# Performance work log

Hardware: AMD Instinct MI355X
Metric: run time of the kernel (lower is better)

Reference implementation:

```python
import jax, jax.numpy as jnp
import numpy as np

N_NODES = 75000
N_EDGES = 1200000
DIM = 64


def setup_inputs() -> dict:
    key = jax.random.key(0)
    ks = jax.random.split(key, 9)
    d_u = jax.random.normal(ks[0], (N_NODES, DIM), dtype=jnp.float32)
    p_u = jax.random.normal(ks[1], (N_NODES, DIM), dtype=jnp.float32)
    s = 1.0 / np.sqrt(DIM)
    w_q = jax.random.normal(ks[2], (DIM, DIM), dtype=jnp.float32) * s
    w_k = jax.random.normal(ks[3], (DIM, DIM), dtype=jnp.float32) * s
    w_v = jax.random.normal(ks[4], (DIM, DIM), dtype=jnp.float32) * s
    e1 = jax.random.normal(ks[5], (DIM,), dtype=jnp.float32) * s
    e2 = jax.random.normal(ks[6], (DIM,), dtype=jnp.float32) * s
    src = jax.random.randint(ks[7], (N_EDGES,), 0, N_NODES, dtype=jnp.int32)
    dst = jax.random.randint(ks[8], (N_EDGES,), 0, N_NODES, dtype=jnp.int32)
    return {"d_u": d_u, "p_u": p_u, "w_q": w_q, "w_k": w_k, "w_v": w_v,
            "e1": e1, "e2": e2, "src": src, "dst": dst}


def reference(d_u, p_u, w_q, w_k, w_v, e1, e2, src, dst):
    n_nodes = d_u.shape[0]
    # per-node edge scores: e1(w_k(p_u)) on src side, e2(w_q(d_u)) on dst side
    h_src = (p_u @ w_k.T) @ e1            # [N]
    h_dst = (d_u @ w_q.T) @ e2            # [N]
    # apply_edges(u_add_v): c_e = h_src[u] + h_dst[v], shape [E]
    c = h_src[src] + h_dst[dst]
    # EdgeWeightNorm(norm='right'): divide by sum of incoming edge weights at dst
    denom = jax.ops.segment_sum(c, dst, num_segments=n_nodes)  # [N]
    c = c / denom[dst]
    # update_all(u_mul_e, sum): messages w_v(p_u)[u] * c_e, summed at dst
    wv = p_u @ w_v.T                      # [N, D]
    msg = wv[src] * c[:, None]            # [E, D]
    out = jax.ops.segment_sum(msg, dst, num_segments=n_nodes)  # [N, D]
    return out
```

## Files before the change

### kernel.cpp

```cpp
#include <hip/hip_runtime.h>

#define N_NODES 75000
#define N_EDGES 1200000
#define DIM 64
#define SCAN_BLK 1024
#define N_SCAN_BLKS ((N_NODES + SCAN_BLK - 1) / SCAN_BLK)
#define NCOPY 8
#define HIST_BLKS ((N_EDGES + 1023) / 1024)

__device__ __forceinline__ float lane_bcf(float v, int l) {
    return __int_as_float(__builtin_amdgcn_readlane(__float_as_int(v), l));
}
__device__ __forceinline__ int lane_bci(int v, int l) {
    return __builtin_amdgcn_readlane(v, l);
}

__global__ void vec_precompute(const float* __restrict__ w_q,
                               const float* __restrict__ w_k,
                               const float* __restrict__ e1,
                               const float* __restrict__ e2,
                               double* __restrict__ a,
                               double* __restrict__ b) {
    int t = threadIdx.x;
    if (t < DIM) {
        double s = 0.0;
        #pragma unroll
        for (int j = 0; j < DIM; ++j) s += (double)e1[j] * (double)w_k[j * DIM + t];
        a[t] = s;
    } else if (t < 2 * DIM) {
        int d = t - DIM;
        double s = 0.0;
        #pragma unroll
        for (int j = 0; j < DIM; ++j) s += (double)e2[j] * (double)w_q[j * DIM + d];
        b[d] = s;
    }
}

__global__ __launch_bounds__(256, 4) void node_wave(
    const float* __restrict__ d_u, const float* __restrict__ p_u,
    const float* __restrict__ w_v,
    const double* __restrict__ a_vec, const double* __restrict__ b_vec,
    double* __restrict__ h_src, double* __restrict__ h_dst,
    float* __restrict__ wv_out) {
    int lane = threadIdx.x & 63;
    int wave = (blockIdx.x * 256 + threadIdx.x) >> 6;
    int nwaves = gridDim.x * 4;

    float w[DIM];
    const float4* wr = (const float4*)(w_v + (size_t)lane * DIM);
    #pragma unroll
    for (int k = 0; k < DIM / 4; ++k) {
        float4 v = wr[k];
        w[4 * k + 0] = v.x; w[4 * k + 1] = v.y;
        w[4 * k + 2] = v.z; w[4 * k + 3] = v.w;
    }
    double al = a_vec[lane];
    double bl = b_vec[lane];

    for (int i = wave; i < N_NODES; i += nwaves) {
        float pl = p_u[(size_t)i * DIM + lane];
        float dl = d_u[(size_t)i * DIM + lane];

        double hs = (double)pl * al;
        #pragma unroll
        for (int off = 32; off > 0; off >>= 1) hs += __shfl_xor(hs, off, 64);
        double hd = (double)dl * bl;
        #pragma unroll
        for (int off = 32; off > 0; off >>= 1) hd += __shfl_xor(hd, off, 64);
        if (lane == 0) { h_src[i] = hs; h_dst[i] = hd; }

        float a0 = 0.f, a1 = 0.f, a2 = 0.f, a3 = 0.f;
        #pragma unroll
        for (int d = 0; d < DIM; d += 4) {
            a0 += w[d + 0] * lane_bcf(pl, d + 0);
            a1 += w[d + 1] * lane_bcf(pl, d + 1);
            a2 += w[d + 2] * lane_bcf(pl, d + 2);
            a3 += w[d + 3] * lane_bcf(pl, d + 3);
        }
        wv_out[(size_t)i * DIM + lane] = (a0 + a1) + (a2 + a3);
    }
}

__global__ __launch_bounds__(256) void hist_kernel(
    const int* __restrict__ dst, int* __restrict__ cnt8,
    int* __restrict__ rank) {
    int base = blockIdx.x << 10;
    int* mycnt = cnt8 + (size_t)(blockIdx.x & (NCOPY - 1)) * N_NODES;
    #pragma unroll
    for (int k = 0; k < 4; ++k) {
        int e = base + k * 256 + threadIdx.x;
        if (e < N_EDGES) rank[e] = atomicAdd(&mycnt[dst[e]], 1);
    }
}

__global__ __launch_bounds__(SCAN_BLK) void scan1_kernel(
    int* __restrict__ cnt8, int* __restrict__ cnt,
    int* __restrict__ row, int* __restrict__ bsum) {
    __shared__ int sh[SCAN_BLK];
    int tid = threadIdx.x;
    int i = blockIdx.x * SCAN_BLK + tid;
    int v = 0;
    if (i < N_NODES) {
        int run = 0;
        #pragma unroll
        for (int c = 0; c < NCOPY; ++c) {
            int x = cnt8[(size_t)c * N_NODES + i];
            cnt8[(size_t)c * N_NODES + i] = run;
            run += x;
        }
        v = run;
        cnt[i] = run;
    }
    sh[tid] = v;
    __syncthreads();
    for (int off = 1; off < SCAN_BLK; off <<= 1) {
        int t = (tid >= off) ? sh[tid - off] : 0;
        __syncthreads();
        sh[tid] += t;
        __syncthreads();
    }
    if (i < N_NODES) row[i] = sh[tid] - v;
    if (tid == SCAN_BLK - 1) bsum[blockIdx.x] = sh[tid];
}

__global__ __launch_bounds__(256) void scan23_kernel(
    int* __restrict__ row, const int* __restrict__ bsum) {
    __shared__ int pref[N_SCAN_BLKS];
    int tid = threadIdx.x;
    if (tid == 0) {
        int run = 0;
        #pragma unroll 8
        for (int k = 0; k < N_SCAN_BLKS; ++k) { pref[k] = run; run += bsum[k]; }
    }
    __syncthreads();
    int i = blockIdx.x * 256 + tid;
    if (i >= N_NODES) return;
    row[i] += pref[i / SCAN_BLK];
}

__global__ __launch_bounds__(256) void build_kernel(
    const int* __restrict__ src, const int* __restrict__ dst,
    const int* __restrict__ row, const int* __restrict__ cnt8,
    const int* __restrict__ rank, int* __restrict__ csr_src) {
    int e = blockIdx.x * 256 + threadIdx.x;
    if (e >= N_EDGES) return;
    int d = dst[e];
    int copy = (e >> 10) & (NCOPY - 1);
    int pos = row[d] + cnt8[(size_t)copy * N_NODES + d] + rank[e];
    csr_src[pos] = src[e];
}

__global__ __launch_bounds__(256) void node_gather(
    const int* __restrict__ row, const int* __restrict__ cnt,
    const int* __restrict__ csr_src,
    const double* __restrict__ h_src, const double* __restrict__ h_dst,
    const float* __restrict__ wv, float* __restrict__ out) {
    int gtid = blockIdx.x * 256 + threadIdx.x;
    int node = gtid >> 6;
    int lane = threadIdx.x & 63;
    if (node >= N_NODES) return;

    int start = row[node];
    int deg = cnt[node];
    double hd = h_dst[node];

    if (deg <= 64) {
        int s0 = 0;
        double c0 = 0.0;
        if (lane < deg) {
            s0 = csr_src[start + lane];
            c0 = h_src[s0] + hd;
        }
        double r = c0;
        if (deg > 32) r += __shfl_xor(r, 32, 64);
        if (deg > 16) r += __shfl_xor(r, 16, 64);
        r += __shfl_xor(r, 8, 64);
        r += __shfl_xor(r, 4, 64);
        r += __shfl_xor(r, 2, 64);
        r += __shfl_xor(r, 1, 64);
        double inv = 1.0 / r;
        float cf0 = (lane < deg) ? (float)(c0 * inv) : 0.f;

        int g = lane >> 4;
        int sub = lane & 15;
        float ax = 0.f, ay = 0.f, az = 0.f, aw = 0.f;
        int rounds = (deg + 3) >> 2;
        int j = 0;
        for (; j + 2 <= rounds; j += 2) {
            int l0 = 4 * j + g;
            int l1 = l0 + 4;
            int   sA = __shfl(s0, l0, 64);
            float cA = __shfl(cf0, l0, 64);
            int   sB = __shfl(s0, l1, 64);
            float cB = __shfl(cf0, l1, 64);
            float4 vA = ((const float4*)(wv + (size_t)sA * DIM))[sub];
            float4 vB = ((const float4*)(wv + (size_t)sB * DIM))[sub];
            ax += vA.x * cA; ay += vA.y * cA; az += vA.z * cA; aw += vA.w * cA;
            ax += vB.x * cB; ay += vB.y * cB; az += vB.z * cB; aw += vB.w * cB;
        }
        if (j < rounds) {
            int l0 = 4 * j + g;
            int   sA = __shfl(s0, l0, 64);
            float cA = __shfl(cf0, l0, 64);
            float4 vA = ((const float4*)(wv + (size_t)sA * DIM))[sub];
            ax += vA.x * cA; ay += vA.y * cA; az += vA.z * cA; aw += vA.w * cA;
        }
        ax += __shfl_xor(ax, 16, 64); ay += __shfl_xor(ay, 16, 64);
        az += __shfl_xor(az, 16, 64); aw += __shfl_xor(aw, 16, 64);
        ax += __shfl_xor(ax, 32, 64); ay += __shfl_xor(ay, 32, 64);
        az += __shfl_xor(az, 32, 64); aw += __shfl_xor(aw, 32, 64);
        if (g == 0) {
            float4 o; o.x = ax; o.y = ay; o.z = az; o.w = aw;
            ((float4*)(out + (size_t)node * DIM))[sub] = o;
        }
    } else {
        double denom = 0.0;
        for (int base = 0; base < deg; base += 64) {
            int m = deg - base; if (m > 64) m = 64;
            double c = 0.0;
            if (lane < m) {
                int s = csr_src[start + base + lane];
                c = h_src[s] + hd;
            }
            #pragma unroll
            for (int off = 32; off > 0; off >>= 1) c += __shfl_xor(c, off, 64);
            denom += c;
        }
        double inv = 1.0 / denom;
        float acc = 0.f;
        for (int base = 0; base < deg; base += 64) {
            int m = deg - base; if (m > 64) m = 64;
            int s1 = 0; float cf1 = 0.f;
            if (lane < m) {
                s1 = csr_src[start + base + lane];
                cf1 = (float)((h_src[s1] + hd) * inv);
            }
            for (int j = 0; j < m; ++j) {
                int s = lane_bci(s1, j);
                float cf = lane_bcf(cf1, j);
                acc += wv[(size_t)s * DIM + lane] * cf;
            }
        }
        out[(size_t)node * DIM + lane] = acc;
    }
}

extern "C" void kernel_launch(void* const* d_in, const int* in_sizes, int n_in,
                              void* d_out, int out_size, void* d_ws, size_t ws_size,
                              hipStream_t stream) {
    const float* d_u = (const float*)d_in[0];
    const float* p_u = (const float*)d_in[1];
    const float* w_q = (const float*)d_in[2];
    const float* w_k = (const float*)d_in[3];
    const float* w_v = (const float*)d_in[4];
    const float* e1  = (const float*)d_in[5];
    const float* e2  = (const float*)d_in[6];
    const int*   src = (const int*)d_in[7];
    const int*   dst = (const int*)d_in[8];
    float* out = (float*)d_out;

    double* a      = (double*)d_ws;
    double* b      = a + DIM;
    double* h_src  = b + DIM;
    double* h_dst  = h_src + N_NODES;
    float*  wv     = (float*)(h_dst + N_NODES);
    int*    cnt    = (int*)(wv + (size_t)N_NODES * DIM);
    int*    row    = cnt + N_NODES;
    int*    bsum   = row + N_NODES;
    int*    cnt8   = bsum + 128;
    int*    rank   = cnt8 + (size_t)NCOPY * N_NODES;
    int*    csr_src= rank + N_EDGES;

    vec_precompute<<<1, 128, 0, stream>>>(w_q, w_k, e1, e2, a, b);

    hipMemsetAsync(cnt8, 0, sizeof(int) * (size_t)NCOPY * N_NODES, stream);

    hist_kernel<<<HIST_BLKS, 256, 0, stream>>>(dst, cnt8, rank);

    node_wave<<<1024, 256, 0, stream>>>(
        d_u, p_u, w_v, a, b, h_src, h_dst, wv);

    scan1_kernel<<<N_SCAN_BLKS, SCAN_BLK, 0, stream>>>(cnt8, cnt, row, bsum);
    scan23_kernel<<<(N_NODES + 255) / 256, 256, 0, stream>>>(row, bsum);

    build_kernel<<<(N_EDGES + 255) / 256, 256, 0, stream>>>(
        src, dst, row, cnt8, rank, csr_src);

    node_gather<<<(N_NODES * 64 + 255) / 256, 256, 0, stream>>>(
        row, cnt, csr_src, h_src, h_dst, wv, out);
}
```

Measured before the change: 255.8 us.

## Fuse histogram, node projection and vector precompute into one launch

Merges the edge histogram kernel and the per-node projection kernel into one grid, with block-index ranges selecting the role. The tiny vec_precompute kernel is removed, and each wave now recomputes its a/b dot-product coefficients inline from w_k, w_q, e1 and e2. This removes two kernel launches and lets the atomic-heavy histogram overlap with the bandwidth-bound node projection. In exchange every node wave does redundant 64-term double-precision reductions, and the histogram blocks now run under the fat kernel's launch bounds and register budget.

```diff
diff --git a/kernel.cpp b/kernel.cpp
--- a/kernel.cpp
+++ b/kernel.cpp
@@ -7,6 +7,8 @@
 #define N_SCAN_BLKS ((N_NODES + SCAN_BLK - 1) / SCAN_BLK)
 #define NCOPY 8
 #define HIST_BLKS ((N_EDGES + 1023) / 1024)
+#define NW_BLKS 1024
+#define FAT_BLKS (HIST_BLKS + NW_BLKS)
 
 __device__ __forceinline__ float lane_bcf(float v, int l) {
     return __int_as_float(__builtin_amdgcn_readlane(__float_as_int(v), l));
@@ -15,36 +17,36 @@
     return __builtin_amdgcn_readlane(v, l);
 }
 
-__global__ void vec_precompute(const float* __restrict__ w_q,
-                               const float* __restrict__ w_k,
-                               const float* __restrict__ e1,
-                               const float* __restrict__ e2,
-                               double* __restrict__ a,
-                               double* __restrict__ b) {
-    int t = threadIdx.x;
-    if (t < DIM) {
-        double s = 0.0;
-        #pragma unroll
-        for (int j = 0; j < DIM; ++j) s += (double)e1[j] * (double)w_k[j * DIM + t];
-        a[t] = s;
-    } else if (t < 2 * DIM) {
-        int d = t - DIM;
-        double s = 0.0;
-        #pragma unroll
-        for (int j = 0; j < DIM; ++j) s += (double)e2[j] * (double)w_q[j * DIM + d];
-        b[d] = s;
-    }
-}
-
-__global__ __launch_bounds__(256, 4) void node_wave(
+__global__ __launch_bounds__(256, 4) void fat_kernel(
+    const int* __restrict__ dst, int* __restrict__ cnt8, int* __restrict__ rank,
     const float* __restrict__ d_u, const float* __restrict__ p_u,
-    const float* __restrict__ w_v,
-    const double* __restrict__ a_vec, const double* __restrict__ b_vec,
+    const float* __restrict__ w_v, const float* __restrict__ w_q,
+    const float* __restrict__ w_k,
+    const float* __restrict__ e1, const float* __restrict__ e2,
     double* __restrict__ h_src, double* __restrict__ h_dst,
     float* __restrict__ wv_out) {
+
+    if (blockIdx.x < HIST_BLKS) {
+        int base = blockIdx.x << 10;
+        int* mycnt = cnt8 + (size_t)(blockIdx.x & (NCOPY - 1)) * N_NODES;
+        #pragma unroll
+        for (int k = 0; k < 4; ++k) {
+            int e = base + k * 256 + threadIdx.x;
+            if (e < N_EDGES) rank[e] = atomicAdd(&mycnt[dst[e]], 1);
+        }
+        return;
+    }
+
     int lane = threadIdx.x & 63;
-    int wave = (blockIdx.x * 256 + threadIdx.x) >> 6;
-    int nwaves = gridDim.x * 4;
+    int wave = ((blockIdx.x - HIST_BLKS) * 256 + threadIdx.x) >> 6;
+    int nwaves = NW_BLKS * 4;
+
+    double al = 0.0, bl = 0.0;
+    #pragma unroll 8
+    for (int j = 0; j < DIM; ++j) {
+        al += (double)e1[j] * (double)w_k[j * DIM + lane];
+        bl += (double)e2[j] * (double)w_q[j * DIM + lane];
+    }
 
     float w[DIM];
     const float4* wr = (const float4*)(w_v + (size_t)lane * DIM);
@@ -54,8 +56,6 @@
         w[4 * k + 0] = v.x; w[4 * k + 1] = v.y;
         w[4 * k + 2] = v.z; w[4 * k + 3] = v.w;
     }
-    double al = a_vec[lane];
-    double bl = b_vec[lane];
 
     for (int i = wave; i < N_NODES; i += nwaves) {
         float pl = p_u[(size_t)i * DIM + lane];
@@ -78,18 +78,6 @@
             a3 += w[d + 3] * lane_bcf(pl, d + 3);
         }
         wv_out[(size_t)i * DIM + lane] = (a0 + a1) + (a2 + a3);
-    }
-}
-
-__global__ __launch_bounds__(256) void hist_kernel(
-    const int* __restrict__ dst, int* __restrict__ cnt8,
-    int* __restrict__ rank) {
-    int base = blockIdx.x << 10;
-    int* mycnt = cnt8 + (size_t)(blockIdx.x & (NCOPY - 1)) * N_NODES;
-    #pragma unroll
-    for (int k = 0; k < 4; ++k) {
-        int e = base + k * 256 + threadIdx.x;
-        if (e < N_EDGES) rank[e] = atomicAdd(&mycnt[dst[e]], 1);
     }
 }
 
@@ -259,9 +247,7 @@
     const int*   dst = (const int*)d_in[8];
     float* out = (float*)d_out;
 
-    double* a      = (double*)d_ws;
-    double* b      = a + DIM;
-    double* h_src  = b + DIM;
+    double* h_src  = (double*)d_ws;
     double* h_dst  = h_src + N_NODES;
     float*  wv     = (float*)(h_dst + N_NODES);
     int*    cnt    = (int*)(wv + (size_t)N_NODES * DIM);
@@ -271,14 +257,10 @@
     int*    rank   = cnt8 + (size_t)NCOPY * N_NODES;
     int*    csr_src= rank + N_EDGES;
 
-    vec_precompute<<<1, 128, 0, stream>>>(w_q, w_k, e1, e2, a, b);
-
     hipMemsetAsync(cnt8, 0, sizeof(int) * (size_t)NCOPY * N_NODES, stream);
 
-    hist_kernel<<<HIST_BLKS, 256, 0, stream>>>(dst, cnt8, rank);
-
-    node_wave<<<1024, 256, 0, stream>>>(
-        d_u, p_u, w_v, a, b, h_src, h_dst, wv);
+    fat_kernel<<<FAT_BLKS, 256, 0, stream>>>(
+        dst, cnt8, rank, d_u, p_u, w_v, w_q, w_k, e1, e2, h_src, h_dst, wv);
 
     scan1_kernel<<<N_SCAN_BLKS, SCAN_BLK, 0, stream>>>(cnt8, cnt, row, bsum);
     scan23_kernel<<<(N_NODES + 255) / 256, 256, 0, stream>>>(row, bsum);
```

New measurement: 254.1 us. No clear change (-0.6%).

## Shard histogram counters by XCC id and parallelize block-prefix scan

Applied to the files above, without the earlier changes.

The histogram kernel now picks its counter copy from the hardware XCC id rather than the block index. Atomics from each XCC then hit a private copy, which is meant to avoid cross-die contention on the same cache lines. The copy index is stored in the upper bits of rank so the build kernel can recover it. Each histogram block also handles twice as many edges, and the single-thread serial prefix over block sums is replaced with a parallel shared-memory scan. This relies on an MI300/MI355 hardware register and on the rank staying below 2^28.

```diff
diff --git a/kernel.cpp b/kernel.cpp
--- a/kernel.cpp
+++ b/kernel.cpp
@@ -6,7 +6,8 @@
 #define SCAN_BLK 1024
 #define N_SCAN_BLKS ((N_NODES + SCAN_BLK - 1) / SCAN_BLK)
 #define NCOPY 8
-#define HIST_BLKS ((N_EDGES + 1023) / 1024)
+#define HIST_EPB 2048
+#define HIST_BLKS ((N_EDGES + HIST_EPB - 1) / HIST_EPB)
 
 __device__ __forceinline__ float lane_bcf(float v, int l) {
     return __int_as_float(__builtin_amdgcn_readlane(__float_as_int(v), l));
@@ -84,12 +85,19 @@
 __global__ __launch_bounds__(256) void hist_kernel(
     const int* __restrict__ dst, int* __restrict__ cnt8,
     int* __restrict__ rank) {
-    int base = blockIdx.x << 10;
-    int* mycnt = cnt8 + (size_t)(blockIdx.x & (NCOPY - 1)) * N_NODES;
+    int xcc;
+    asm("s_getreg_b32 %0, hwreg(HW_REG_XCC_ID)" : "=s"(xcc));
+    xcc &= (NCOPY - 1);
+    int* mycnt = cnt8 + (size_t)xcc * N_NODES;
+    int tag = xcc << 28;
+    int base = blockIdx.x * HIST_EPB;
     #pragma unroll
-    for (int k = 0; k < 4; ++k) {
+    for (int k = 0; k < HIST_EPB / 256; ++k) {
         int e = base + k * 256 + threadIdx.x;
-        if (e < N_EDGES) rank[e] = atomicAdd(&mycnt[dst[e]], 1);
+        if (e < N_EDGES) {
+            int r = atomicAdd(&mycnt[dst[e]], 1);
+            rank[e] = r | tag;
+        }
     }
 }
 
@@ -125,13 +133,23 @@
 
 __global__ __launch_bounds__(256) void scan23_kernel(
     int* __restrict__ row, const int* __restrict__ bsum) {
-    __shared__ int pref[N_SCAN_BLKS];
+    __shared__ int pref[128];
     int tid = threadIdx.x;
-    if (tid == 0) {
-        int run = 0;
-        #pragma unroll 8
-        for (int k = 0; k < N_SCAN_BLKS; ++k) { pref[k] = run; run += bsum[k]; }
-    }
+    int v = 0;
+    if (tid < 128) {
+        v = (tid < N_SCAN_BLKS) ? bsum[tid] : 0;
+        pref[tid] = v;
+    }
+    __syncthreads();
+    #pragma unroll
+    for (int off = 1; off < 128; off <<= 1) {
+        int t = 0;
+        if (tid < 128 && tid >= off) t = pref[tid - off];
+        __syncthreads();
+        if (tid < 128) pref[tid] += t;
+        __syncthreads();
+    }
+    if (tid < 128) pref[tid] -= v;
     __syncthreads();
     int i = blockIdx.x * 256 + tid;
     if (i >= N_NODES) return;
@@ -145,8 +163,10 @@
     int e = blockIdx.x * 256 + threadIdx.x;
     if (e >= N_EDGES) return;
     int d = dst[e];
-    int copy = (e >> 10) & (NCOPY - 1);
-    int pos = row[d] + cnt8[(size_t)copy * N_NODES + d] + rank[e];
+    int rp = rank[e];
+    int copy = (rp >> 28) & (NCOPY - 1);
+    int r = rp & 0x0FFFFFFF;
+    int pos = row[d] + cnt8[(size_t)copy * N_NODES + d] + r;
     csr_src[pos] = src[e];
 }
 
```

After: 263.3 us. 2.9% more time.

## Use per-XCC histogram copies and fuse the scan with a decoupled lookback

Applied to the files above, without the earlier changes.

The histogram kernel now picks its counter copy from the hardware XCC id instead of the block index. It uses relaxed workgroup-scope atomics and packs the copy tag into the high bits of each rank, so atomic traffic stays within one XCC's L2. The two-pass scan becomes a single kernel: each block publishes its flagged block sum and spins on its predecessors' sums, which removes one launch. The CSR build uses nontemporal stores, and the memset is widened to also clear the publish flags. The risks are that workgroup-scope atomics across blocks depend on XCC-local L2 coherence, and that the spin-wait depends on earlier blocks being scheduled first.

```diff
diff --git a/kernel.cpp b/kernel.cpp
--- a/kernel.cpp
+++ b/kernel.cpp
@@ -36,6 +36,27 @@
     }
 }
 
+__global__ __launch_bounds__(256) void hist_kernel(
+    const int* __restrict__ dst, int* __restrict__ cnt8,
+    int* __restrict__ rank) {
+    int xcc;
+    asm volatile("s_getreg_b32 %0, hwreg(HW_REG_XCC_ID)" : "=s"(xcc));
+    xcc &= (NCOPY - 1);
+    int* mycnt = cnt8 + (size_t)xcc * N_NODES;
+    int tag = xcc << 28;
+    int base = blockIdx.x << 10;
+    #pragma unroll
+    for (int k = 0; k < 4; ++k) {
+        int e = base + k * 256 + threadIdx.x;
+        if (e < N_EDGES) {
+            int r = __hip_atomic_fetch_add(&mycnt[dst[e]], 1,
+                                           __ATOMIC_RELAXED,
+                                           __HIP_MEMORY_SCOPE_WORKGROUP);
+            rank[e] = r | tag;
+        }
+    }
+}
+
 __global__ __launch_bounds__(256, 4) void node_wave(
     const float* __restrict__ d_u, const float* __restrict__ p_u,
     const float* __restrict__ w_v,
@@ -81,22 +102,11 @@
     }
 }
 
-__global__ __launch_bounds__(256) void hist_kernel(
-    const int* __restrict__ dst, int* __restrict__ cnt8,
-    int* __restrict__ rank) {
-    int base = blockIdx.x << 10;
-    int* mycnt = cnt8 + (size_t)(blockIdx.x & (NCOPY - 1)) * N_NODES;
-    #pragma unroll
-    for (int k = 0; k < 4; ++k) {
-        int e = base + k * 256 + threadIdx.x;
-        if (e < N_EDGES) rank[e] = atomicAdd(&mycnt[dst[e]], 1);
-    }
-}
-
-__global__ __launch_bounds__(SCAN_BLK) void scan1_kernel(
+__global__ __launch_bounds__(SCAN_BLK) void scan_kernel(
     int* __restrict__ cnt8, int* __restrict__ cnt,
-    int* __restrict__ row, int* __restrict__ bsum) {
+    int* __restrict__ row, unsigned int* __restrict__ pub) {
     __shared__ int sh[SCAN_BLK];
+    __shared__ int bpref;
     int tid = threadIdx.x;
     int i = blockIdx.x * SCAN_BLK + tid;
     int v = 0;
@@ -119,23 +129,22 @@
         sh[tid] += t;
         __syncthreads();
     }
-    if (i < N_NODES) row[i] = sh[tid] - v;
-    if (tid == SCAN_BLK - 1) bsum[blockIdx.x] = sh[tid];
-}
-
-__global__ __launch_bounds__(256) void scan23_kernel(
-    int* __restrict__ row, const int* __restrict__ bsum) {
-    __shared__ int pref[N_SCAN_BLKS];
-    int tid = threadIdx.x;
-    if (tid == 0) {
-        int run = 0;
-        #pragma unroll 8
-        for (int k = 0; k < N_SCAN_BLKS; ++k) { pref[k] = run; run += bsum[k]; }
+    int incl = sh[tid];
+    if (tid == SCAN_BLK - 1)
+        atomicExch(&pub[blockIdx.x], (unsigned)incl | 0x80000000u);
+    if (tid < 64) {
+        int s = 0;
+        for (int l = tid; l < (int)blockIdx.x; l += 64) {
+            unsigned x;
+            do { x = atomicAdd(&pub[l], 0u); } while (!(x & 0x80000000u));
+            s += (int)(x & 0x7FFFFFFFu);
+        }
+        #pragma unroll
+        for (int off = 32; off > 0; off >>= 1) s += __shfl_xor(s, off, 64);
+        if (tid == 0) bpref = s;
     }
     __syncthreads();
-    int i = blockIdx.x * 256 + tid;
-    if (i >= N_NODES) return;
-    row[i] += pref[i / SCAN_BLK];
+    if (i < N_NODES) row[i] = bpref + incl - v;
 }
 
 __global__ __launch_bounds__(256) void build_kernel(
@@ -145,9 +154,11 @@
     int e = blockIdx.x * 256 + threadIdx.x;
     if (e >= N_EDGES) return;
     int d = dst[e];
-    int copy = (e >> 10) & (NCOPY - 1);
-    int pos = row[d] + cnt8[(size_t)copy * N_NODES + d] + rank[e];
-    csr_src[pos] = src[e];
+    int rp = rank[e];
+    int copy = (rp >> 28) & (NCOPY - 1);
+    int r = rp & 0x0FFFFFFF;
+    int pos = row[d] + cnt8[(size_t)copy * N_NODES + d] + r;
+    __builtin_nontemporal_store(src[e], &csr_src[pos]);
 }
 
 __global__ __launch_bounds__(256) void node_gather(
@@ -266,22 +277,22 @@
     float*  wv     = (float*)(h_dst + N_NODES);
     int*    cnt    = (int*)(wv + (size_t)N_NODES * DIM);
     int*    row    = cnt + N_NODES;
-    int*    bsum   = row + N_NODES;
-    int*    cnt8   = bsum + 128;
-    int*    rank   = cnt8 + (size_t)NCOPY * N_NODES;
+    int*    cnt8   = row + N_NODES;
+    unsigned int* pub = (unsigned int*)(cnt8 + (size_t)NCOPY * N_NODES);
+    int*    rank   = (int*)pub + 128;
     int*    csr_src= rank + N_EDGES;
 
+    hipMemsetAsync(cnt8, 0, sizeof(int) * ((size_t)NCOPY * N_NODES + 128),
+                   stream);
+
     vec_precompute<<<1, 128, 0, stream>>>(w_q, w_k, e1, e2, a, b);
-
-    hipMemsetAsync(cnt8, 0, sizeof(int) * (size_t)NCOPY * N_NODES, stream);
 
     hist_kernel<<<HIST_BLKS, 256, 0, stream>>>(dst, cnt8, rank);
 
     node_wave<<<1024, 256, 0, stream>>>(
         d_u, p_u, w_v, a, b, h_src, h_dst, wv);
 
-    scan1_kernel<<<N_SCAN_BLKS, SCAN_BLK, 0, stream>>>(cnt8, cnt, row, bsum);
-    scan23_kernel<<<(N_NODES + 255) / 256, 256, 0, stream>>>(row, bsum);
+    scan_kernel<<<N_SCAN_BLKS, SCAN_BLK, 0, stream>>>(cnt8, cnt, row, pub);
 
     build_kernel<<<(N_EDGES + 255) / 256, 256, 0, stream>>>(
         src, dst, row, cnt8, rank, csr_src);
```

Measured after the change: 267.1 us. 1.04x slower.
